# Kernel optimization log

Measured on AMD Instinct MI355X. Metric: run time of the kernel, lower is better.

The kernel has to match this reference:

```python
import jax, jax.numpy as jnp
import numpy as np


def _l2norm(x, eps=1e-12):
    # F.normalize(dim=-1): x / max(||x||, eps)
    n = jnp.sqrt(jnp.sum(x * x, axis=-1, keepdims=True))
    return x / jnp.maximum(n, eps)


def setup_inputs() -> dict:
    key = jax.random.key(0)
    k1, k2, k3 = jax.random.split(key, 3)
    B, L, D = 4, 8192, 1024
    x = jax.random.normal(k1, (B, L, D), dtype=jnp.float32)
    # RoutingModule initializes q_proj/k_proj to identity; perturb slightly so the
    # projections are exercised but boundary probabilities stay realistic.
    Wq = jnp.eye(D, dtype=jnp.float32) + 0.02 * jax.random.normal(k2, (D, D), jnp.float32)
    Wk = jnp.eye(D, dtype=jnp.float32) + 0.02 * jax.random.normal(k3, (D, D), jnp.float32)
    return {"x": x, "Wq": Wq, "Wk": Wk, "chunk_divisor": 4}


def reference(x, Wq, Wk, chunk_divisor):
    B, L, D = x.shape
    max_chunks = L // chunk_divisor

    # ---- RoutingModule: p_t = 0.5*(1 - cos(q_t, k_{t-1})), p_0 = 1 ----
    q = _l2norm(jnp.einsum('bld,ed->ble', x[:, 1:], Wq))   # [B, L-1, D]
    k = _l2norm(jnp.einsum('bld,ed->ble', x[:, :-1], Wk))  # [B, L-1, D]
    cos_sim = jnp.einsum('bld,bld->bl', q, k)
    p = jnp.clip((1.0 - cos_sim) * 0.5, 0.0, 1.0)
    p = jnp.concatenate([jnp.ones((B, 1), p.dtype), p], axis=1)  # [B, L]
    boundary_mask = p >= 0.5

    # ---- ChunkLayer: gather boundary positions to the front, right-pad ----
    num_chunks = jnp.minimum(jnp.sum(boundary_mask, axis=-1), max_chunks)  # [B]
    token_idx = jnp.arange(L)[None, :] + (~boundary_mask).astype(jnp.int32) * L
    sorted_idx = jnp.argsort(token_idx, axis=1)
    take_idx = sorted_idx[:, :max_chunks]                                   # [B, C]
    chunked = jnp.take_along_axis(x, take_idx[:, :, None], axis=1)          # [B, C, D]
    pad_mask = jnp.arange(max_chunks)[None, :] < num_chunks[:, None]        # [B, C]
    chunked = chunked * pad_mask[:, :, None].astype(chunked.dtype)

    # ---- DeChunkLayer: EMA smoothing via associative scan, then scatter back ----
    C = max_chunks
    p_chunked = jnp.take_along_axis(p, take_idx, axis=1)
    p_chunked = jnp.clip(p_chunked, 1e-4, 1.0 - 1e-4)                       # [B, C]
    decay = jnp.broadcast_to((1.0 - p_chunked)[:, :, None], chunked.shape)  # [B, C, D]
    weighted_x = p_chunked[:, :, None] * chunked
    decay = decay.at[:, 0].set(0.0)
    weighted_x = weighted_x.at[:, 0].set(chunked[:, 0])

    def combine(left, right):
        d_l, v_l = left
        d_r, v_r = right
        return (d_l * d_r, v_r + d_r * v_l)

    _, smoothed = jax.lax.associative_scan(combine, (decay, weighted_x), axis=1)

    chunk_id = jnp.clip(jnp.cumsum(boundary_mask.astype(jnp.int32), axis=1) - 1, 0, C - 1)
    out = jnp.take_along_axis(smoothed, chunk_id[:, :, None], axis=1)       # [B, L, D]
    return out
```

## Files before the change

### kernel.cpp

```cpp
#include <hip/hip_runtime.h>
#include <math.h>

#define B_ 4
#define L_ 8192
#define D_ 1024
#define C_ 2048
#define CG 128
#define NG (C_/CG)
#define TAUF 3.0e-4f
#define MAXF 4096
#define FXF 8

typedef unsigned short ushortt;
using f32x4  = __attribute__((ext_vector_type(4))) float;
using bf16x8 = __attribute__((ext_vector_type(8))) short;

__device__ __forceinline__ ushortt f2bf(float f) {
    unsigned int u = __float_as_uint(f);
    u = (u + 0x7fffu + ((u >> 16) & 1u)) >> 16;
    return (ushortt)u;
}
__device__ __forceinline__ float bf2f(ushortt h) {
    return __uint_as_float(((unsigned int)h) << 16);
}

#define GLOAD16(gsrc, ldst) \
    __builtin_amdgcn_global_load_lds( \
        (const __attribute__((address_space(1))) unsigned int*)(gsrc), \
        (__attribute__((address_space(3))) unsigned int*)(ldst), 16, 0, 0)

__global__ __launch_bounds__(256) void k_prep(
    const float* __restrict__ Wq, const float* __restrict__ Wk,
    ushortt* __restrict__ eqb, ushortt* __restrict__ ekb)
{
    const float* W = blockIdx.y ? Wk : Wq;
    ushortt* E = blockIdx.y ? ekb : eqb;
    size_t i8 = ((size_t)blockIdx.x * 256 + threadIdx.x) * 8;
    int e = (int)(i8 >> 10), k0 = (int)(i8 & 1023);
    float4 a = *(const float4*)&W[i8];
    float4 b = *(const float4*)&W[i8 + 4];
    float v[8] = {a.x, a.y, a.z, a.w, b.x, b.y, b.z, b.w};
    ushortt o[8];
#pragma unroll
    for (int j = 0; j < 8; ++j) {
        float t = v[j] - ((k0 + j == e) ? 1.0f : 0.0f);
        o[j] = f2bf(t);
    }
    *(uint4*)&E[i8] = *(uint4*)o;
}

__global__ __launch_bounds__(256) void k_xb(
    const float* __restrict__ x, ushortt* __restrict__ xb)
{
    size_t i8 = ((size_t)blockIdx.x * 256 + threadIdx.x) * 8;
    float4 a = *(const float4*)&x[i8];
    float4 b = *(const float4*)&x[i8 + 4];
    float v[8] = {a.x, a.y, a.z, a.w, b.x, b.y, b.z, b.w};
    ushortt o[8];
#pragma unroll
    for (int j = 0; j < 8; ++j) o[j] = f2bf(v[j]);
    *(uint4*)&xb[i8] = *(uint4*)o;
}

__global__ __launch_bounds__(512) void k_gemm(
    const ushortt* __restrict__ xb, const ushortt* __restrict__ eqb,
    const ushortt* __restrict__ ekb,
    float* __restrict__ p, int* __restrict__ cnt, int* __restrict__ flags)
{
    __shared__ ushortt xsh[2][129 * 32];
    __shared__ ushortt eqsh[2][128 * 32];
    __shared__ ushortt eksh[2][128 * 32];
    __shared__ float part[128][4];

    const int tid = threadIdx.x;
    const int b = blockIdx.y;
    const int t0 = blockIdx.x * 128;
    const int lane = tid & 63;
    const int w = tid >> 6;
    const int wr = w & 3, wc = w >> 2;
    const int l15 = lane & 15, lg = lane >> 4;

    const int tq = tid & 255;
    const ushortt* egl = (tid < 256) ? eqb : ekb;

    float nq[8], nk[8], dt[8];
#pragma unroll
    for (int i = 0; i < 8; ++i) { nq[i] = 0.f; nk[i] = 0.f; dt[i] = 0.f; }

    f32x4 acc[2][8];
#pragma unroll
    for (int rb = 0; rb < 2; ++rb)
#pragma unroll
        for (int f = 0; f < 8; ++f) acc[rb][f] = (f32x4){0.f, 0.f, 0.f, 0.f};

    auto stage = [&](int it, int buf) {
        const int kb = it & 31, nb = it >> 5;
        const int k0 = kb * 32, e0 = nb * 128;
        uint4 extra;
        if (tid < 4)
            extra = *(const uint4*)&xb[((size_t)b * L_ + (t0 + 127)) * D_ + k0 + tid * 8];
        {
            int row = tid >> 2, g = tid & 3;
            int trow = t0 - 1 + row; if (trow < 0) trow = 0;
            const ushortt* src = &xb[((size_t)b * L_ + trow) * D_ + k0 + g * 8];
            GLOAD16(src, &xsh[buf][tid * 8]);
        }
        ushortt* edst = (tid < 256) ? eqsh[buf] : eksh[buf];
#pragma unroll
        for (int r = 0; r < 2; ++r) {
            int row = r * 64 + (tq >> 2), g = tq & 3;
            const ushortt* src = &egl[(size_t)(e0 + row) * D_ + k0 + g * 8];
            GLOAD16(src, &edst[r * 2048 + tq * 8]);
        }
        if (tid < 4)
            *(uint4*)&xsh[buf][128 * 32 + tid * 8] = extra;
    };

    stage(0, 0);
    __syncthreads();

    int buf = 0;
    for (int it = 0; it < 256; ++it) {
        if (it + 1 < 256) stage(it + 1, buf ^ 1);
        const ushortt* xsb = xsh[buf];
        const ushortt* eqs = eqsh[buf];
        const ushortt* eks = eksh[buf];
        {
            const int kk = lg * 8;
            bf16x8 aq[2], ak[2], bq[4], bk[4];
#pragma unroll
            for (int rb = 0; rb < 2; ++rb) {
                int rq = 1 + wr * 32 + rb * 16 + l15;
                int rk = rq - 1;
                aq[rb] = *(const bf16x8*)&xsb[rq * 32 + kk];
                ak[rb] = *(const bf16x8*)&xsb[rk * 32 + kk];
            }
#pragma unroll
            for (int cf = 0; cf < 4; ++cf) {
                int er = wc * 64 + cf * 16 + l15;
                int off = er * 32 + kk;
                bq[cf] = *(const bf16x8*)&eqs[off];
                bk[cf] = *(const bf16x8*)&eks[off];
            }
#pragma unroll
            for (int rb = 0; rb < 2; ++rb)
#pragma unroll
                for (int cf = 0; cf < 4; ++cf) {
                    acc[rb][cf]     = __builtin_amdgcn_mfma_f32_16x16x32_bf16(aq[rb], bq[cf], acc[rb][cf],     0, 0, 0);
                    acc[rb][cf + 4] = __builtin_amdgcn_mfma_f32_16x16x32_bf16(ak[rb], bk[cf], acc[rb][cf + 4], 0, 0, 0);
                }
        }
        if ((it & 31) == 31) {
            const int e0 = (it >> 5) * 128;
#pragma unroll
            for (int rb = 0; rb < 2; ++rb)
#pragma unroll
                for (int cf = 0; cf < 4; ++cf) {
                    const int ecol = e0 + wc * 64 + cf * 16 + l15;
                    const int tb = t0 + wr * 32 + rb * 16 + lg * 4;
                    const ushortt* xc = &xb[((size_t)b * L_ + tb) * D_ + ecol];
                    float xt0 = bf2f(xc[0]), xt1 = bf2f(xc[D_]);
                    float xt2 = bf2f(xc[2 * D_]), xt3 = bf2f(xc[3 * D_]);
                    float xm0 = (tb == 0) ? xt0 : bf2f(xc[-(int)D_]);
                    float xtv[4] = {xt0, xt1, xt2, xt3};
                    float xmv[4] = {xm0, xt0, xt1, xt2};
#pragma unroll
                    for (int r = 0; r < 4; ++r) {
                        float qe = xtv[r] + acc[rb][cf][r];
                        float ke = xmv[r] + acc[rb][cf + 4][r];
                        const int s = rb * 4 + r;
                        nq[s] = fmaf(qe, qe, nq[s]);
                        nk[s] = fmaf(ke, ke, nk[s]);
                        dt[s] = fmaf(qe, ke, dt[s]);
                    }
                }
#pragma unroll
            for (int rb = 0; rb < 2; ++rb)
#pragma unroll
                for (int f = 0; f < 8; ++f) acc[rb][f] = (f32x4){0.f, 0.f, 0.f, 0.f};
        }
        __syncthreads();
        buf ^= 1;
    }

#pragma unroll
    for (int m = 1; m < 16; m <<= 1) {
#pragma unroll
        for (int s = 0; s < 8; ++s) {
            nq[s] += __shfl_xor(nq[s], m);
            nk[s] += __shfl_xor(nk[s], m);
            dt[s] += __shfl_xor(dt[s], m);
        }
    }
    if (wc == 1 && l15 == 0) {
#pragma unroll
        for (int s = 0; s < 8; ++s) {
            int rl = wr * 32 + (s >> 2) * 16 + lg * 4 + (s & 3);
            part[rl][0] = nq[s]; part[rl][1] = nk[s]; part[rl][2] = dt[s];
        }
    }
    __syncthreads();
    if (wc == 0 && l15 == 0) {
#pragma unroll
        for (int s = 0; s < 8; ++s) {
            int rl = wr * 32 + (s >> 2) * 16 + lg * 4 + (s & 3);
            int t = t0 + rl;
            float a = nq[s] + part[rl][0];
            float c = nk[s] + part[rl][1];
            float d = dt[s] + part[rl][2];
            float qn = fmaxf(sqrtf(a), 1e-12f);
            float kn = fmaxf(sqrtf(c), 1e-12f);
            float cs = d / (qn * kn);
            float pv = fminf(fmaxf((1.0f - cs) * 0.5f, 0.0f), 1.0f);
            if (t == 0) pv = 1.0f;
            p[b * L_ + t] = pv;
            if (t > 0 && fabsf(cs) < TAUF) {
                int idx = atomicAdd(cnt, 1);
                if (idx < MAXF) flags[idx] = b * L_ + t;
            }
        }
    }
}

__global__ __launch_bounds__(256) void k_fix(
    const float* __restrict__ x, const float* __restrict__ Wq,
    const float* __restrict__ Wk, const int* __restrict__ cnt,
    const int* __restrict__ flags, float* __restrict__ parts)
{
    int n = *cnt; if (n > MAXF) n = MAXF;
    const int m0 = blockIdx.x * FXF;
    if (m0 >= n) return;
    const int e0 = blockIdx.y * 128;

    __shared__ float xs[FXF * 2][1024];
    __shared__ float ws[2][128 * 17];
    __shared__ float comb[FXF * 4][128];
    __shared__ float red2[2][FXF][3];

    const int tid = threadIdx.x;
    const int e = tid & 127;
    const int kh = tid >> 7;

    {
        int row = tid >> 4, c0 = (tid & 15) * 64;
        int f = row >> 1, wh = row & 1;
        int sl = m0 + f;
        int gf = flags[(sl < n) ? sl : m0];
        int fb = gf >> 13, ft = (gf & (L_ - 1)) - wh;
        const float* src = &x[((size_t)fb * L_ + ft) * D_ + c0];
#pragma unroll
        for (int i = 0; i < 16; ++i)
            *(float4*)&xs[row][c0 + i * 4] = *(const float4*)&src[i * 4];
    }

    const int sr = tid >> 1, sk = (tid & 1) * 8;
    const float* gWq = &Wq[(size_t)(e0 + sr) * D_ + sk];
    const float* gWk = &Wk[(size_t)(e0 + sr) * D_ + sk];

    float acc[FXF][2];
#pragma unroll
    for (int f = 0; f < FXF; ++f) { acc[f][0] = 0.f; acc[f][1] = 0.f; }

    float4 pq0 = ((const float4*)gWq)[0], pq1 = ((const float4*)gWq)[1];
    float4 pk0 = ((const float4*)gWk)[0], pk1 = ((const float4*)gWk)[1];

    for (int kc = 0; kc < 64; ++kc) {
        __syncthreads();
        {
            int o = sr * 17 + sk;
            ws[0][o + 0] = pq0.x; ws[0][o + 1] = pq0.y; ws[0][o + 2] = pq0.z; ws[0][o + 3] = pq0.w;
            ws[0][o + 4] = pq1.x; ws[0][o + 5] = pq1.y; ws[0][o + 6] = pq1.z; ws[0][o + 7] = pq1.w;
            ws[1][o + 0] = pk0.x; ws[1][o + 1] = pk0.y; ws[1][o + 2] = pk0.z; ws[1][o + 3] = pk0.w;
            ws[1][o + 4] = pk1.x; ws[1][o + 5] = pk1.y; ws[1][o + 6] = pk1.z; ws[1][o + 7] = pk1.w;
        }
        if (kc + 1 < 64) {
            const float* nq2 = gWq + (kc + 1) * 16;
            const float* nk2 = gWk + (kc + 1) * 16;
            pq0 = ((const float4*)nq2)[0]; pq1 = ((const float4*)nq2)[1];
            pk0 = ((const float4*)nk2)[0]; pk1 = ((const float4*)nk2)[1];
        }
        __syncthreads();
        float wq[8], wk[8];
#pragma unroll
        for (int j = 0; j < 8; ++j) {
            wq[j] = ws[0][e * 17 + kh * 8 + j];
            wk[j] = ws[1][e * 17 + kh * 8 + j];
        }
        const int kbase = kc * 16 + kh * 8;
#pragma unroll
        for (int f = 0; f < FXF; ++f) {
            float aq = acc[f][0], ak = acc[f][1];
#pragma unroll
            for (int j2 = 0; j2 < 2; ++j2) {
                float4 xq = *(const float4*)&xs[f * 2][kbase + j2 * 4];
                float4 xk = *(const float4*)&xs[f * 2 + 1][kbase + j2 * 4];
                aq = fmaf(xq.x, wq[j2 * 4 + 0], aq); aq = fmaf(xq.y, wq[j2 * 4 + 1], aq);
                aq = fmaf(xq.z, wq[j2 * 4 + 2], aq); aq = fmaf(xq.w, wq[j2 * 4 + 3], aq);
                ak = fmaf(xk.x, wk[j2 * 4 + 0], ak); ak = fmaf(xk.y, wk[j2 * 4 + 1], ak);
                ak = fmaf(xk.z, wk[j2 * 4 + 2], ak); ak = fmaf(xk.w, wk[j2 * 4 + 3], ak);
            }
            acc[f][0] = aq; acc[f][1] = ak;
        }
    }

    __syncthreads();
#pragma unroll
    for (int f = 0; f < FXF; ++f) {
        comb[(f * 2 + 0) * 2 + kh][e] = acc[f][0];
        comb[(f * 2 + 1) * 2 + kh][e] = acc[f][1];
    }
    __syncthreads();
    if (tid < 128) {
        float r0[FXF], r1[FXF], r2[FXF];
#pragma unroll
        for (int f = 0; f < FXF; ++f) {
            float q = comb[(f * 2 + 0) * 2 + 0][e] + comb[(f * 2 + 0) * 2 + 1][e];
            float k = comb[(f * 2 + 1) * 2 + 0][e] + comb[(f * 2 + 1) * 2 + 1][e];
            r0[f] = q * q; r1[f] = k * k; r2[f] = q * k;
        }
#pragma unroll
        for (int m = 1; m < 64; m <<= 1) {
#pragma unroll
            for (int f = 0; f < FXF; ++f) {
                r0[f] += __shfl_xor(r0[f], m);
                r1[f] += __shfl_xor(r1[f], m);
                r2[f] += __shfl_xor(r2[f], m);
            }
        }
        if ((tid & 63) == 0) {
            int wv = tid >> 6;
#pragma unroll
            for (int f = 0; f < FXF; ++f) {
                red2[wv][f][0] = r0[f]; red2[wv][f][1] = r1[f]; red2[wv][f][2] = r2[f];
            }
        }
    }
    __syncthreads();
    if (tid < FXF) {
        float A  = red2[0][tid][0] + red2[1][tid][0];
        float Cc = red2[0][tid][1] + red2[1][tid][1];
        float Dd = red2[0][tid][2] + red2[1][tid][2];
        if (m0 + tid < n) {
            size_t o = ((size_t)(m0 + tid) * 8 + blockIdx.y) * 3;
            parts[o] = A; parts[o + 1] = Cc; parts[o + 2] = Dd;
        }
    }
}

__global__ __launch_bounds__(256) void k_fix_final(
    const int* __restrict__ cnt, const int* __restrict__ flags,
    const float* __restrict__ parts, float* __restrict__ p)
{
    int n = *cnt; if (n > MAXF) n = MAXF;
    int f = blockIdx.x * 256 + threadIdx.x;
    if (f >= n) return;
    float a = 0.f, c = 0.f, d = 0.f;
#pragma unroll
    for (int e = 0; e < 8; ++e) {
        size_t o = ((size_t)f * 8 + e) * 3;
        a += parts[o + 0]; c += parts[o + 1]; d += parts[o + 2];
    }
    float qn = fmaxf(sqrtf(a), 1e-12f);
    float kn = fmaxf(sqrtf(c), 1e-12f);
    float cs = d / (qn * kn);
    float pv = fminf(fmaxf((1.0f - cs) * 0.5f, 0.0f), 1.0f);
    p[flags[f]] = pv;
}

__global__ __launch_bounds__(1024) void k_boundaries(
    const float* __restrict__ p, int* __restrict__ take, int* __restrict__ nch,
    float2* __restrict__ cw, int* __restrict__ segev)
{
    const int b = blockIdx.x;
    const int tid = threadIdx.x;
    __shared__ int ssum[1024];
    __shared__ int tl[C_];

    bool m[8];
    int local = 0;
#pragma unroll
    for (int j = 0; j < 8; ++j) {
        int l = tid * 8 + j;
        m[j] = (p[b * L_ + l] >= 0.5f);
        local += m[j] ? 1 : 0;
    }
    ssum[tid] = local;
    __syncthreads();
    for (int off = 1; off < 1024; off <<= 1) {
        int add = (tid >= off) ? ssum[tid - off] : 0;
        __syncthreads();
        ssum[tid] += add;
        __syncthreads();
    }
    const int total = ssum[1023];
    int rank = ssum[tid] - local;
#pragma unroll
    for (int j = 0; j < 8; ++j) {
        if (m[j]) {
            if (rank < C_) { take[b * C_ + rank] = tid * 8 + j; tl[rank] = tid * 8 + j; }
            ++rank;
        }
    }
    const int K = (total < C_) ? total : C_;
    if (tid == 0) nch[b] = K;
    for (int c = total + tid; c < C_; c += 1024) { take[b * C_ + c] = 0; tl[c] = 0; }
    __syncthreads();
    for (int c = tid; c < C_; c += 1024) {
        int idx = tl[c];
        float pc = p[b * L_ + idx];
        pc = fminf(fmaxf(pc, 1e-4f), 1.f - 1e-4f);
        float dc = (c == 0) ? 0.f : (1.f - pc);
        float wv = (c == 0) ? 1.f : pc;
        cw[b * C_ + c] = make_float2(dc, wv);
        segev[b * C_ + c] = (c + 1 < K) ? tl[c + 1] : L_;
    }
}

__global__ __launch_bounds__(256) void k_scan_local(
    const float* __restrict__ x, const int* __restrict__ take,
    const float2* __restrict__ cw, float* __restrict__ E, float* __restrict__ M)
{
    const int g = blockIdx.x, b = blockIdx.y, zq = blockIdx.z;
    const int d = zq * 256 + threadIdx.x;
    const int base = b * C_ + g * CG;

    float s = 0.f, mm = 1.f;
    for (int cc = 0; cc < CG; cc += 4) {
        int4 i4 = *(const int4*)&take[base + cc];
        float2 w0 = cw[base + cc], w1 = cw[base + cc + 1];
        float2 w2 = cw[base + cc + 2], w3 = cw[base + cc + 3];
        float x0 = x[((size_t)b * L_ + i4.x) * D_ + d];
        float x1 = x[((size_t)b * L_ + i4.y) * D_ + d];
        float x2 = x[((size_t)b * L_ + i4.z) * D_ + d];
        float x3 = x[((size_t)b * L_ + i4.w) * D_ + d];
        s = fmaf(w0.x, s, w0.y * x0); mm *= w0.x;
        s = fmaf(w1.x, s, w1.y * x1); mm *= w1.x;
        s = fmaf(w2.x, s, w2.y * x2); mm *= w2.x;
        s = fmaf(w3.x, s, w3.y * x3); mm *= w3.x;
    }
    E[((size_t)b * NG + g) * D_ + d] = s;
    if (threadIdx.x == 0 && zq == 0) M[b * NG + g] = mm;
}

__global__ __launch_bounds__(256) void k_scan_groups(
    const float* __restrict__ E, const float* __restrict__ M, float* __restrict__ carry)
{
    const int gid = blockIdx.x * 256 + threadIdx.x;
    const int b = gid >> 10, d = gid & 1023;
    float s = 0.f;
    for (int g = 0; g < NG; ++g) {
        carry[((size_t)b * NG + g) * D_ + d] = s;
        s = E[((size_t)b * NG + g) * D_ + d] + M[b * NG + g] * s;
    }
}

__global__ __launch_bounds__(256) void k_scan_out(
    const float* __restrict__ x, const int* __restrict__ take,
    const float2* __restrict__ cw, const int* __restrict__ segev,
    const int* __restrict__ nch, const float* __restrict__ carry,
    float* __restrict__ last_s, float* __restrict__ out)
{
    const int g = blockIdx.x, b = blockIdx.y, zq = blockIdx.z;
    const int d = zq * 256 + threadIdx.x;
    const int K = nch[b];
    const int c0 = g * CG;
    if (c0 >= K) return;
    const int c1 = (c0 + CG < K) ? (c0 + CG) : K;
    const int base = b * C_;

    float s = carry[((size_t)b * NG + g) * D_ + d];
    int idx = take[base + c0];
    float2 w0 = cw[base + c0];
    float xv = x[((size_t)b * L_ + idx) * D_ + d];
    for (int c = c0; c < c1; ++c) {
        int idxn = 0; float2 wn = make_float2(0.f, 0.f); float xn = 0.f;
        if (c + 1 < c1) {
            idxn = take[base + c + 1];
            wn = cw[base + c + 1];
            xn = x[((size_t)b * L_ + idxn) * D_ + d];
        }
        s = fmaf(w0.x, s, w0.y * xv);
        if (c == K - 1) {
            last_s[b * D_ + d] = s;
        } else {
            int sege = segev[base + c];
            for (int l = idx; l < sege; ++l)
                out[((size_t)b * L_ + l) * D_ + d] = s;
        }
        idx = idxn; w0 = wn; xv = xn;
    }
}

__global__ __launch_bounds__(256) void k_tail(
    const int* __restrict__ take, const int* __restrict__ nch,
    const float* __restrict__ last_s, float* __restrict__ out)
{
    const int b = blockIdx.y;
    const int tt0 = blockIdx.x * 8;
    const int K = nch[b];
    const int start = take[b * C_ + K - 1];
    if (tt0 + 8 <= start) return;
    float4 v = *(const float4*)&last_s[b * D_ + threadIdx.x * 4];
#pragma unroll
    for (int j = 0; j < 8; ++j) {
        int t = tt0 + j;
        if (t >= start)
            *(float4*)&out[((size_t)b * L_ + t) * D_ + threadIdx.x * 4] = v;
    }
}

extern "C" void kernel_launch(void* const* d_in, const int* in_sizes, int n_in,
                              void* d_out, int out_size, void* d_ws, size_t ws_size,
                              hipStream_t stream)
{
    (void)in_sizes; (void)n_in; (void)out_size;
    const float* x  = (const float*)d_in[0];
    const float* Wq = (const float*)d_in[1];
    const float* Wk = (const float*)d_in[2];
    float* out = (float*)d_out;

    char* ws = (char*)d_ws;
    float*  p      = (float*)(ws + 0);
    int*    take   = (int*)  (ws + 131072);
    int*    nch    = (int*)  (ws + 163840);
    float*  M      = (float*)(ws + 164096);
    float2* cw     = (float2*)(ws + 164608);
    int*    segev  = (int*)  (ws + 230144);
    float*  last_s = (float*)(ws + 262912);
    int*    cnt    = (int*)  (ws + 279296);
    int*    flags  = (int*)  (ws + 279552);
    float*  parts  = (float*)(ws + 295936);
    float*  E      = (float*)(ws + 689152);
    float*  carry  = (float*)(ws + 951296);
    ushortt* eqb   = (ushortt*)(ws + 1213440);
    ushortt* ekb   = (ushortt*)(ws + 3310592);
    if (ws_size < 5407744u) return;

    ushortt* xb = (ushortt*)d_out;

    hipMemsetAsync(cnt, 0, 256, stream);
    k_prep<<<dim3(512, 2), 256, 0, stream>>>(Wq, Wk, eqb, ekb);
    k_xb<<<16384, 256, 0, stream>>>(x, xb);
    k_gemm<<<dim3(64, B_), 512, 0, stream>>>(xb, eqb, ekb, p, cnt, flags);
    k_fix<<<dim3(MAXF / FXF, 8), 256, 0, stream>>>(x, Wq, Wk, cnt, flags, parts);
    k_fix_final<<<MAXF / 256, 256, 0, stream>>>(cnt, flags, parts, p);
    k_boundaries<<<B_, 1024, 0, stream>>>(p, take, nch, cw, segev);
    dim3 g3(NG, B_, 4);
    k_scan_local<<<g3, 256, 0, stream>>>(x, take, cw, E, M);
    k_scan_groups<<<(B_ * D_) / 256, 256, 0, stream>>>(E, M, carry);
    k_scan_out<<<g3, 256, 0, stream>>>(x, take, cw, segev, nch, carry, last_s, out);
    k_tail<<<dim3(L_ / 8, B_), 256, 0, stream>>>(take, nch, last_s, out);
}
```

Baseline: 501.6 us.

## Widen GEMM N-tile to 256 with 2x4 wave layout and swizzled LDS

The fused q/k projection GEMM now processes 256 output columns per stage instead of 128, with waves arranged 2 rows by 4 columns, each covering a 64x64 tile for both q and k. This raises MFMA work per LDS load of the x tile and halves the number of K-loop stages. An XOR swizzle is added to the LDS layout of the x and E tiles to cut bank conflicts on the bf16x8 reads. The final norm and dot reduction now gathers four column partials through shared memory. The cost is more accumulator registers and more LDS per block, which can lower occupancy.

After: 442.9 us. 1.13x faster.

```diff
diff --git a/kernel.cpp b/kernel.cpp
--- a/kernel.cpp
+++ b/kernel.cpp
@@ -29,6 +29,8 @@
         (const __attribute__((address_space(1))) unsigned int*)(gsrc), \
         (__attribute__((address_space(3))) unsigned int*)(ldst), 16, 0, 0)
 
+__device__ __forceinline__ int swz32(int row, int g) { return g ^ ((row >> 1) & 3); }
+
 __global__ __launch_bounds__(256) void k_prep(
     const float* __restrict__ Wq, const float* __restrict__ Wk,
     ushortt* __restrict__ eqb, ushortt* __restrict__ ekb)
@@ -68,48 +70,52 @@
     float* __restrict__ p, int* __restrict__ cnt, int* __restrict__ flags)
 {
     __shared__ ushortt xsh[2][129 * 32];
-    __shared__ ushortt eqsh[2][128 * 32];
-    __shared__ ushortt eksh[2][128 * 32];
-    __shared__ float part[128][4];
+    __shared__ ushortt eqsh[2][256 * 32];
+    __shared__ ushortt eksh[2][256 * 32];
+    __shared__ float part[128][4][3];
 
     const int tid = threadIdx.x;
     const int b = blockIdx.y;
     const int t0 = blockIdx.x * 128;
     const int lane = tid & 63;
     const int w = tid >> 6;
-    const int wr = w & 3, wc = w >> 2;
+    const int wr = w >> 2;
+    const int wc = w & 3;
     const int l15 = lane & 15, lg = lane >> 4;
 
     const int tq = tid & 255;
     const ushortt* egl = (tid < 256) ? eqb : ekb;
 
-    float nq[8], nk[8], dt[8];
-#pragma unroll
-    for (int i = 0; i < 8; ++i) { nq[i] = 0.f; nk[i] = 0.f; dt[i] = 0.f; }
-
-    f32x4 acc[2][8];
-#pragma unroll
-    for (int rb = 0; rb < 2; ++rb)
-#pragma unroll
-        for (int f = 0; f < 8; ++f) acc[rb][f] = (f32x4){0.f, 0.f, 0.f, 0.f};
+    float nq[16], nk[16], dt[16];
+#pragma unroll
+    for (int i = 0; i < 16; ++i) { nq[i] = 0.f; nk[i] = 0.f; dt[i] = 0.f; }
+
+    f32x4 aqa[4][4], aka[4][4];
+#pragma unroll
+    for (int rb = 0; rb < 4; ++rb)
+#pragma unroll
+        for (int cf = 0; cf < 4; ++cf) {
+            aqa[rb][cf] = (f32x4){0.f, 0.f, 0.f, 0.f};
+            aka[rb][cf] = (f32x4){0.f, 0.f, 0.f, 0.f};
+        }
 
     auto stage = [&](int it, int buf) {
         const int kb = it & 31, nb = it >> 5;
-        const int k0 = kb * 32, e0 = nb * 128;
+        const int k0 = kb * 32, e0 = nb * 256;
         uint4 extra;
         if (tid < 4)
             extra = *(const uint4*)&xb[((size_t)b * L_ + (t0 + 127)) * D_ + k0 + tid * 8];
         {
             int row = tid >> 2, g = tid & 3;
             int trow = t0 - 1 + row; if (trow < 0) trow = 0;
-            const ushortt* src = &xb[((size_t)b * L_ + trow) * D_ + k0 + g * 8];
+            const ushortt* src = &xb[((size_t)b * L_ + trow) * D_ + k0 + swz32(row, g) * 8];
             GLOAD16(src, &xsh[buf][tid * 8]);
         }
         ushortt* edst = (tid < 256) ? eqsh[buf] : eksh[buf];
 #pragma unroll
-        for (int r = 0; r < 2; ++r) {
+        for (int r = 0; r < 4; ++r) {
             int row = r * 64 + (tq >> 2), g = tq & 3;
-            const ushortt* src = &egl[(size_t)(e0 + row) * D_ + k0 + g * 8];
+            const ushortt* src = &egl[(size_t)(e0 + row) * D_ + k0 + swz32(row, g) * 8];
             GLOAD16(src, &edst[r * 2048 + tq * 8]);
         }
         if (tid < 4)
@@ -120,44 +126,42 @@
     __syncthreads();
 
     int buf = 0;
-    for (int it = 0; it < 256; ++it) {
-        if (it + 1 < 256) stage(it + 1, buf ^ 1);
+    for (int it = 0; it < 128; ++it) {
+        if (it + 1 < 128) stage(it + 1, buf ^ 1);
         const ushortt* xsb = xsh[buf];
         const ushortt* eqs = eqsh[buf];
         const ushortt* eks = eksh[buf];
         {
-            const int kk = lg * 8;
-            bf16x8 aq[2], ak[2], bq[4], bk[4];
-#pragma unroll
-            for (int rb = 0; rb < 2; ++rb) {
-                int rq = 1 + wr * 32 + rb * 16 + l15;
+            bf16x8 aq[4], ak[4];
+#pragma unroll
+            for (int rb = 0; rb < 4; ++rb) {
+                int rq = 1 + wr * 64 + rb * 16 + l15;
                 int rk = rq - 1;
-                aq[rb] = *(const bf16x8*)&xsb[rq * 32 + kk];
-                ak[rb] = *(const bf16x8*)&xsb[rk * 32 + kk];
+                aq[rb] = *(const bf16x8*)&xsb[rq * 32 + swz32(rq, lg) * 8];
+                ak[rb] = *(const bf16x8*)&xsb[rk * 32 + swz32(rk, lg) * 8];
             }
 #pragma unroll
             for (int cf = 0; cf < 4; ++cf) {
                 int er = wc * 64 + cf * 16 + l15;
-                int off = er * 32 + kk;
-                bq[cf] = *(const bf16x8*)&eqs[off];
-                bk[cf] = *(const bf16x8*)&eks[off];
+                int off = er * 32 + swz32(er, lg) * 8;
+                bf16x8 bq = *(const bf16x8*)&eqs[off];
+#pragma unroll
+                for (int rb = 0; rb < 4; ++rb)
+                    aqa[rb][cf] = __builtin_amdgcn_mfma_f32_16x16x32_bf16(aq[rb], bq, aqa[rb][cf], 0, 0, 0);
+                bf16x8 bk = *(const bf16x8*)&eks[off];
+#pragma unroll
+                for (int rb = 0; rb < 4; ++rb)
+                    aka[rb][cf] = __builtin_amdgcn_mfma_f32_16x16x32_bf16(ak[rb], bk, aka[rb][cf], 0, 0, 0);
             }
-#pragma unroll
-            for (int rb = 0; rb < 2; ++rb)
-#pragma unroll
-                for (int cf = 0; cf < 4; ++cf) {
-                    acc[rb][cf]     = __builtin_amdgcn_mfma_f32_16x16x32_bf16(aq[rb], bq[cf], acc[rb][cf],     0, 0, 0);
-                    acc[rb][cf + 4] = __builtin_amdgcn_mfma_f32_16x16x32_bf16(ak[rb], bk[cf], acc[rb][cf + 4], 0, 0, 0);
-                }
         }
         if ((it & 31) == 31) {
-            const int e0 = (it >> 5) * 128;
-#pragma unroll
-            for (int rb = 0; rb < 2; ++rb)
+            const int e0 = (it >> 5) * 256;
+#pragma unroll
+            for (int rb = 0; rb < 4; ++rb)
 #pragma unroll
                 for (int cf = 0; cf < 4; ++cf) {
                     const int ecol = e0 + wc * 64 + cf * 16 + l15;
-                    const int tb = t0 + wr * 32 + rb * 16 + lg * 4;
+                    const int tb = t0 + wr * 64 + rb * 16 + lg * 4;
                     const ushortt* xc = &xb[((size_t)b * L_ + tb) * D_ + ecol];
                     float xt0 = bf2f(xc[0]), xt1 = bf2f(xc[D_]);
                     float xt2 = bf2f(xc[2 * D_]), xt3 = bf2f(xc[3 * D_]);
@@ -166,8 +170,8 @@
                     float xmv[4] = {xm0, xt0, xt1, xt2};
 #pragma unroll
                     for (int r = 0; r < 4; ++r) {
-                        float qe = xtv[r] + acc[rb][cf][r];
-                        float ke = xmv[r] + acc[rb][cf + 4][r];
+                        float qe = xtv[r] + aqa[rb][cf][r];
+                        float ke = xmv[r] + aka[rb][cf][r];
                         const int s = rb * 4 + r;
                         nq[s] = fmaf(qe, qe, nq[s]);
                         nk[s] = fmaf(ke, ke, nk[s]);
@@ -175,9 +179,12 @@
                     }
                 }
 #pragma unroll
-            for (int rb = 0; rb < 2; ++rb)
-#pragma unroll
-                for (int f = 0; f < 8; ++f) acc[rb][f] = (f32x4){0.f, 0.f, 0.f, 0.f};
+            for (int rb = 0; rb < 4; ++rb)
+#pragma unroll
+                for (int cf = 0; cf < 4; ++cf) {
+                    aqa[rb][cf] = (f32x4){0.f, 0.f, 0.f, 0.f};
+                    aka[rb][cf] = (f32x4){0.f, 0.f, 0.f, 0.f};
+                }
         }
         __syncthreads();
         buf ^= 1;
@@ -186,38 +193,36 @@
 #pragma unroll
     for (int m = 1; m < 16; m <<= 1) {
 #pragma unroll
-        for (int s = 0; s < 8; ++s) {
+        for (int s = 0; s < 16; ++s) {
             nq[s] += __shfl_xor(nq[s], m);
             nk[s] += __shfl_xor(nk[s], m);
             dt[s] += __shfl_xor(dt[s], m);
         }
     }
-    if (wc == 1 && l15 == 0) {
-#pragma unroll
-        for (int s = 0; s < 8; ++s) {
-            int rl = wr * 32 + (s >> 2) * 16 + lg * 4 + (s & 3);
-            part[rl][0] = nq[s]; part[rl][1] = nk[s]; part[rl][2] = dt[s];
-        }
-    }
-    __syncthreads();
-    if (wc == 0 && l15 == 0) {
-#pragma unroll
-        for (int s = 0; s < 8; ++s) {
-            int rl = wr * 32 + (s >> 2) * 16 + lg * 4 + (s & 3);
-            int t = t0 + rl;
-            float a = nq[s] + part[rl][0];
-            float c = nk[s] + part[rl][1];
-            float d = dt[s] + part[rl][2];
-            float qn = fmaxf(sqrtf(a), 1e-12f);
-            float kn = fmaxf(sqrtf(c), 1e-12f);
-            float cs = d / (qn * kn);
-            float pv = fminf(fmaxf((1.0f - cs) * 0.5f, 0.0f), 1.0f);
-            if (t == 0) pv = 1.0f;
-            p[b * L_ + t] = pv;
-            if (t > 0 && fabsf(cs) < TAUF) {
-                int idx = atomicAdd(cnt, 1);
-                if (idx < MAXF) flags[idx] = b * L_ + t;
-            }
+    if (l15 == 0) {
+#pragma unroll
+        for (int s = 0; s < 16; ++s) {
+            int rl = wr * 64 + (s >> 2) * 16 + lg * 4 + (s & 3);
+            part[rl][wc][0] = nq[s];
+            part[rl][wc][1] = nk[s];
+            part[rl][wc][2] = dt[s];
+        }
+    }
+    __syncthreads();
+    if (tid < 128) {
+        int t = t0 + tid;
+        float a = part[tid][0][0] + part[tid][1][0] + part[tid][2][0] + part[tid][3][0];
+        float c = part[tid][0][1] + part[tid][1][1] + part[tid][2][1] + part[tid][3][1];
+        float d = part[tid][0][2] + part[tid][1][2] + part[tid][2][2] + part[tid][3][2];
+        float qn = fmaxf(sqrtf(a), 1e-12f);
+        float kn = fmaxf(sqrtf(c), 1e-12f);
+        float cs = d / (qn * kn);
+        float pv = fminf(fmaxf((1.0f - cs) * 0.5f, 0.0f), 1.0f);
+        if (t == 0) pv = 1.0f;
+        p[b * L_ + t] = pv;
+        if (t > 0 && fabsf(cs) < TAUF) {
+            int idx = atomicAdd(cnt, 1);
+            if (idx < MAXF) flags[idx] = b * L_ + t;
         }
     }
 }
```
